# Kernel optimization log

Hardware: AMD Instinct MI355X
Metric: run time of the kernel (lower is better)

The kernel has to match this reference:

```python
import jax, jax.numpy as jnp
import numpy as np

N_U, N_M = 60000, 20000
F_U, F_M = 64, 128
IN_C, HID, OUT_C = 256, 256, 128
N = N_U + N_M
E = 500000
BN_EPS = 1e-5


def gcn_conv(z, W, b, src, dst, n):
    # PyG GCNConv: h = z @ W; add self-loops; symmetric norm D^-1/2 (A+I) D^-1/2; scatter-add; + bias
    h = z @ W                                        # [n, out]
    loop = jnp.arange(n)
    src_sl = jnp.concatenate([src, loop])            # [E+n]
    dst_sl = jnp.concatenate([dst, loop])
    deg = jax.ops.segment_sum(jnp.ones_like(dst_sl, h.dtype), dst_sl, num_segments=n)
    dinv = jax.lax.rsqrt(deg)                        # deg >= 1 due to self-loops
    norm = dinv[src_sl] * dinv[dst_sl]               # [E+n]
    msg = h[src_sl] * norm[:, None]                  # gather + scale
    out = jax.ops.segment_sum(msg, dst_sl, num_segments=n)
    return out + b


def batch_norm(z, gamma, beta):
    mean = jnp.mean(z, axis=0)
    var = jnp.var(z, axis=0)                         # biased, as torch BN uses for normalization
    return (z - mean) * jax.lax.rsqrt(var + BN_EPS) * gamma + beta


def setup_inputs() -> dict:
    key = jax.random.key(0)
    ks = jax.random.split(key, 13)
    x = jax.random.normal(ks[0], (N_U, F_U), jnp.float32)
    y = jax.random.normal(ks[1], (N_M, F_M), jnp.float32)
    edge_index = jax.random.randint(ks[2], (2, E), 0, N, dtype=jnp.int64)
    def lin(k, fin, fout):
        s = 1.0 / np.sqrt(fin)
        kw, kb = jax.random.split(k)
        return (jax.random.uniform(kw, (fin, fout), jnp.float32, -s, s),
                jax.random.uniform(kb, (fout,), jnp.float32, -s, s))
    fc1_w, fc1_b = lin(ks[3], F_U, IN_C)
    fc2_w, fc2_b = lin(ks[4], F_M, IN_C)
    conv1_w, conv1_b = lin(ks[5], IN_C, HID)
    conv2_w, conv2_b = lin(ks[6], HID, OUT_C)
    bn_gamma = jnp.ones((HID,), jnp.float32)
    bn_beta = jnp.zeros((HID,), jnp.float32)
    return {"x": x, "y": y, "edge_index": edge_index,
            "fc1_w": fc1_w, "fc1_b": fc1_b, "fc2_w": fc2_w, "fc2_b": fc2_b,
            "conv1_w": conv1_w, "conv1_b": conv1_b, "conv2_w": conv2_w, "conv2_b": conv2_b,
            "bn_gamma": bn_gamma, "bn_beta": bn_beta}


def reference(x, y, edge_index, fc1_w, fc1_b, fc2_w, fc2_b,
              conv1_w, conv1_b, conv2_w, conv2_b, bn_gamma, bn_beta):
    src, dst = edge_index[0], edge_index[1]
    xu = x @ fc1_w + fc1_b                           # [N_U, IN_C]
    xm = y @ fc2_w + fc2_b                           # [N_M, IN_C]
    z = jnp.concatenate([xu, xm], axis=0)            # [N, IN_C]
    z = gcn_conv(z, conv1_w, conv1_b, src, dst, N)   # [N, HID]
    z = jax.nn.relu(batch_norm(z, bn_gamma, bn_beta))
    z = gcn_conv(z, conv2_w, conv2_b, src, dst, N)   # [N, OUT_C]
    return z
```

## Files before the change

### kernel.cpp

```cpp
#include <hip/hip_runtime.h>
#include <math.h>
#include <stdint.h>

#define N_U 60000
#define N_M 20000
#define NN  80000
#define EE  500000
#define BN_EPS 1e-5f
#define NB_SCAN 313

typedef __attribute__((ext_vector_type(8))) short short8v;
typedef __attribute__((ext_vector_type(4))) float f32x4;

__device__ __forceinline__ unsigned short bf_hi(float f) {
    unsigned u = __float_as_uint(f);
    return (unsigned short)((u + 0x7FFFu + ((u >> 16) & 1u)) >> 16);
}
__device__ __forceinline__ float bf_f(unsigned short h) {
    return __uint_as_float(((unsigned)h) << 16);
}

__global__ void prep_kernel(const int* __restrict__ ei32, int* __restrict__ cnt,
                            int* __restrict__ cursor, int* __restrict__ rowptr,
                            float* __restrict__ sums, float* __restrict__ sumsq,
                            int* __restrict__ flag) {
    int i = blockIdx.x * blockDim.x + threadIdx.x;
    if (i < 256) { sums[i] = 0.f; sumsq[i] = 0.f; }
    for (int j = i; j < NN; j += gridDim.x * blockDim.x) { cnt[j] = 0; cursor[j] = 0; }
    if (i == 0) rowptr[NN] = EE;
    if (blockIdx.x == 0) {
        __shared__ int nz;
        if (threadIdx.x == 0) nz = 0;
        __syncthreads();
        int v = ei32[2 * threadIdx.x + 1];
        if (v != 0) atomicOr(&nz, 1);
        __syncthreads();
        if (threadIdx.x == 0) *flag = (nz == 0) ? 1 : 0;
    }
}

__device__ __forceinline__ int load_idx(const void* ei, int f, int pos) {
    return f ? (int)((const long long*)ei)[pos] : ((const int*)ei)[pos];
}

__global__ void hist_kernel(const void* __restrict__ ei, const int* __restrict__ flag,
                            int* __restrict__ cnt) {
    int f = *flag;
    int stride = gridDim.x * blockDim.x;
    for (int e = blockIdx.x * blockDim.x + threadIdx.x; e < EE; e += stride) {
        int d = load_idx(ei, f, EE + e);
        atomicAdd(&cnt[d], 1);
    }
}

__global__ void scan1_kernel(const int* __restrict__ cnt, int* __restrict__ rowptr,
                             int* __restrict__ blockSums, float* __restrict__ dinv) {
    __shared__ int sh[256];
    int tid = threadIdx.x;
    int i = blockIdx.x * 256 + tid;
    int v = (i < NN) ? cnt[i] : 0;
    int x = v;
    sh[tid] = x; __syncthreads();
#pragma unroll
    for (int off = 1; off < 256; off <<= 1) {
        int t = (tid >= off) ? sh[tid - off] : 0;
        __syncthreads();
        x += t; sh[tid] = x;
        __syncthreads();
    }
    if (i < NN) {
        rowptr[i] = x - v;
        dinv[i] = rsqrtf(1.0f + (float)v);
    }
    if (tid == 255) blockSums[blockIdx.x] = x;
}

__global__ void scan2_kernel(int* __restrict__ blockSums) {
    __shared__ int sh[512];
    int tid = threadIdx.x;
    int v = (tid < NB_SCAN) ? blockSums[tid] : 0;
    int x = v;
    sh[tid] = x; __syncthreads();
#pragma unroll
    for (int off = 1; off < 512; off <<= 1) {
        int t = (tid >= off) ? sh[tid - off] : 0;
        __syncthreads();
        x += t; sh[tid] = x;
        __syncthreads();
    }
    if (tid < NB_SCAN) blockSums[tid] = x - v;
}

__global__ void scan3_kernel(int* __restrict__ rowptr, const int* __restrict__ blockSums) {
    int i = blockIdx.x * 256 + threadIdx.x;
    if (i < NN) rowptr[i] += blockSums[blockIdx.x];
}

__global__ void fill_kernel(const void* __restrict__ ei, const int* __restrict__ flag,
                            const int* __restrict__ rowptr, int* __restrict__ cursor,
                            int* __restrict__ csr_src) {
    int f = *flag;
    int stride = gridDim.x * blockDim.x;
    for (int e = blockIdx.x * blockDim.x + threadIdx.x; e < EE; e += stride) {
        int s = load_idx(ei, f, e);
        int d = load_idx(ei, f, EE + e);
        int pos = rowptr[d] + atomicAdd(&cursor[d], 1);
        csr_src[pos] = s;
    }
}

__device__ __forceinline__ void wfrag_store(const float* W, short* Hi, short* Lo,
                                            int i, int K, int N) {
    int k = i / N, n = i - k * N;
    float v = W[i];
    unsigned short h = bf_hi(v);
    unsigned short l = bf_hi(v - bf_f(h));
    int nt = n >> 4, r = n & 15, kt = k >> 5, q = (k >> 3) & 3, p = k & 7;
    int idx = ((nt * (K / 32) + kt) << 9) + (q << 7) + (r << 3) + p;
    Hi[idx] = (short)h;
    Lo[idx] = (short)l;
}

__global__ void wsplit_all_kernel(const float* __restrict__ W1, const float* __restrict__ W2,
                                  const float* __restrict__ Wf1, const float* __restrict__ Wf2,
                                  short* __restrict__ W1h, short* __restrict__ W1l,
                                  short* __restrict__ W2h, short* __restrict__ W2l,
                                  short* __restrict__ F1h, short* __restrict__ F1l,
                                  short* __restrict__ F2h, short* __restrict__ F2l) {
    int i = blockIdx.x * 256 + threadIdx.x;
    if (i < 256 * 256) wfrag_store(W1, W1h, W1l, i, 256, 256);
    if (i < 256 * 128) wfrag_store(W2, W2h, W2l, i, 256, 128);
    if (i < 64 * 256)  wfrag_store(Wf1, F1h, F1l, i, 64, 256);
    if (i < 128 * 256) wfrag_store(Wf2, F2h, F2l, i, 128, 256);
}

template <int K, int N, int MODE, int AIN, bool BNRELU, int OUTK>
__global__ __launch_bounds__(256) void mfma_gemm_kernel(
    int M, const float* __restrict__ A,
    const short* __restrict__ AHi, const short* __restrict__ ALo,
    const short* __restrict__ WfHi, const short* __restrict__ WfLo,
    const float* __restrict__ ep, const float* __restrict__ bnsc,
    const float* __restrict__ bnsh,
    float* __restrict__ Out, short* __restrict__ OutB, short* __restrict__ OutL) {
    constexpr int LDT = 40;
    constexpr int NT = K / 32;
    __shared__ short AsHi[128 * LDT];
    __shared__ short AsLo[128 * LDT];
    const int tid  = threadIdx.x;
    const int lane = tid & 63, wave = tid >> 6;
    const int wm = (wave >> 1) * 64, wn = (wave & 1) * 64;
    const int R0 = blockIdx.x * 128;
    const int n0 = blockIdx.y * 128;
    const int srow  = tid >> 1;
    const int shalf = (tid & 1) * 16;
    const int l15  = lane & 15;
    const int koff = (lane >> 4) * 8;
    const int nt0  = (n0 + wn) >> 4;

    f32x4 acc[4][4];
#pragma unroll
    for (int mi = 0; mi < 4; ++mi)
#pragma unroll
        for (int ni = 0; ni < 4; ++ni)
            acc[mi][ni] = (f32x4){0.f, 0.f, 0.f, 0.f};

    const int arow = min(R0 + srow, M - 1);
    const float* abase = (AIN == 0) ? &A[(size_t)arow * K + shalf] : nullptr;
    const short* ahb   = (AIN == 1) ? &AHi[(size_t)arow * K + shalf] : nullptr;
    const short* alb   = (AIN == 1) ? &ALo[(size_t)arow * K + shalf] : nullptr;

    float4 a0, a1, a2, a3;
    int4 th0, th1, tl0, tl1;
    if constexpr (AIN == 0) {
        const float4* ga = (const float4*)abase;
        a0 = ga[0]; a1 = ga[1]; a2 = ga[2]; a3 = ga[3];
    } else {
        th0 = ((const int4*)ahb)[0]; th1 = ((const int4*)ahb)[1];
        tl0 = ((const int4*)alb)[0]; tl1 = ((const int4*)alb)[1];
    }

#pragma unroll
    for (int kt = 0; kt < NT; ++kt) {
        const int k0 = kt * 32;
        int4 sh0, sh1, sl0, sl1;

        if constexpr (AIN == 0) {
            if (BNRELU) {
                const float4* gs = (const float4*)&bnsc[k0 + shalf];
                const float4* gh = (const float4*)&bnsh[k0 + shalf];
                float4 s0 = gs[0], s1 = gs[1], s2 = gs[2], s3 = gs[3];
                float4 t0 = gh[0], t1 = gh[1], t2 = gh[2], t3 = gh[3];
#define BNR4(a, s, t)                                                          \
                a.x = fmaxf(a.x * s.x + t.x, 0.f);                             \
                a.y = fmaxf(a.y * s.y + t.y, 0.f);                             \
                a.z = fmaxf(a.z * s.z + t.z, 0.f);                             \
                a.w = fmaxf(a.w * s.w + t.w, 0.f);
                BNR4(a0, s0, t0); BNR4(a1, s1, t1); BNR4(a2, s2, t2); BNR4(a3, s3, t3);
#undef BNR4
            }
            unsigned h[8], l[8];
#define SPLIT4(v, hA, hB, lA, lB)                                              \
            {                                                                  \
                unsigned short h0_ = bf_hi(v.x), h1_ = bf_hi(v.y);             \
                unsigned short h2_ = bf_hi(v.z), h3_ = bf_hi(v.w);             \
                unsigned short l0_ = bf_hi(v.x - bf_f(h0_));                   \
                unsigned short l1_ = bf_hi(v.y - bf_f(h1_));                   \
                unsigned short l2_ = bf_hi(v.z - bf_f(h2_));                   \
                unsigned short l3_ = bf_hi(v.w - bf_f(h3_));                   \
                hA = (unsigned)h0_ | ((unsigned)h1_ << 16);                    \
                hB = (unsigned)h2_ | ((unsigned)h3_ << 16);                    \
                lA = (unsigned)l0_ | ((unsigned)l1_ << 16);                    \
                lB = (unsigned)l2_ | ((unsigned)l3_ << 16);                    \
            }
            SPLIT4(a0, h[0], h[1], l[0], l[1]);
            SPLIT4(a1, h[2], h[3], l[2], l[3]);
            SPLIT4(a2, h[4], h[5], l[4], l[5]);
            SPLIT4(a3, h[6], h[7], l[6], l[7]);
#undef SPLIT4
            sh0 = make_int4((int)h[0], (int)h[1], (int)h[2], (int)h[3]);
            sh1 = make_int4((int)h[4], (int)h[5], (int)h[6], (int)h[7]);
            sl0 = make_int4((int)l[0], (int)l[1], (int)l[2], (int)l[3]);
            sl1 = make_int4((int)l[4], (int)l[5], (int)l[6], (int)l[7]);
        } else {
            sh0 = th0; sh1 = th1; sl0 = tl0; sl1 = tl1;
        }

        __syncthreads();
        int4* dAH = (int4*)&AsHi[srow * LDT + shalf];
        int4* dAL = (int4*)&AsLo[srow * LDT + shalf];
        dAH[0] = sh0; dAH[1] = sh1;
        dAL[0] = sl0; dAL[1] = sl1;
        __syncthreads();

        if (kt + 1 < NT) {
            if constexpr (AIN == 0) {
                const float4* gnext = (const float4*)(abase + (kt + 1) * 32);
                a0 = gnext[0]; a1 = gnext[1]; a2 = gnext[2]; a3 = gnext[3];
            } else {
                const int4* gh = (const int4*)(ahb + (kt + 1) * 32);
                const int4* gl = (const int4*)(alb + (kt + 1) * 32);
                th0 = gh[0]; th1 = gh[1]; tl0 = gl[0]; tl1 = gl[1];
            }
        }

        short8v bh[4], bl[4];
#pragma unroll
        for (int ni = 0; ni < 4; ++ni) {
            int fidx = (((nt0 + ni) * NT + kt) << 9) + lane * 8;
            bh[ni] = *(const short8v*)&WfHi[fidx];
            bl[ni] = *(const short8v*)&WfLo[fidx];
        }

#pragma unroll
        for (int mi = 0; mi < 4; ++mi) {
            int mrow = wm + mi * 16 + l15;
            short8v ah = *(const short8v*)&AsHi[mrow * LDT + koff];
            short8v al = *(const short8v*)&AsLo[mrow * LDT + koff];
#pragma unroll
            for (int ni = 0; ni < 4; ++ni) {
                acc[mi][ni] = __builtin_amdgcn_mfma_f32_16x16x32_bf16(ah, bh[ni], acc[mi][ni], 0, 0, 0);
                acc[mi][ni] = __builtin_amdgcn_mfma_f32_16x16x32_bf16(ah, bl[ni], acc[mi][ni], 0, 0, 0);
                acc[mi][ni] = __builtin_amdgcn_mfma_f32_16x16x32_bf16(al, bh[ni], acc[mi][ni], 0, 0, 0);
            }
        }
    }

#pragma unroll
    for (int mi = 0; mi < 4; ++mi) {
#pragma unroll
        for (int i = 0; i < 4; ++i) {
            int row = R0 + wm + mi * 16 + (lane >> 4) * 4 + i;
            if (row < M) {
                float sc = (MODE == 0) ? ep[row] : 1.0f;
#pragma unroll
                for (int ni = 0; ni < 4; ++ni) {
                    int col = n0 + wn + ni * 16 + l15;
                    float v = acc[mi][ni][i];
                    v = (MODE == 0) ? v * sc : v + ep[col];
                    if constexpr (OUTK == 0) {
                        Out[(size_t)row * N + col] = v;
                    } else if constexpr (OUTK == 1) {
                        OutB[(size_t)row * N + col] = (short)bf_hi(v);
                    } else {
                        unsigned short h = bf_hi(v);
                        OutB[(size_t)row * N + col] = (short)h;
                        OutL[(size_t)row * N + col] = (short)bf_hi(v - bf_f(h));
                    }
                }
            }
        }
    }
}

__device__ __forceinline__ void acc_bf4(float4& a, ushort4 v) {
    a.x += bf_f(v.x); a.y += bf_f(v.y); a.z += bf_f(v.z); a.w += bf_f(v.w);
}

__global__ __launch_bounds__(256) void gather256_kernel(const short* __restrict__ h,
                                                        const float* __restrict__ bias,
                                                        const float* __restrict__ dinv,
                                                        const int* __restrict__ rowptr,
                                                        const int* __restrict__ csr_src,
                                                        float* __restrict__ out) {
    int wid = threadIdx.x >> 6, lane = threadIdx.x & 63;
    int r = blockIdx.x * 4 + wid;
    if (r >= NN) return;
    int beg = rowptr[r], end = rowptr[r + 1];
    float dr = dinv[r];
    const ushort4* hp = (const ushort4*)h;
    float4 acc = {0.f, 0.f, 0.f, 0.f};
    acc_bf4(acc, hp[(size_t)r * 64 + lane]);
    int k = beg;
    for (; k + 3 < end; k += 4) {
        int s0 = csr_src[k], s1 = csr_src[k + 1], s2 = csr_src[k + 2], s3 = csr_src[k + 3];
        ushort4 v0 = hp[(size_t)s0 * 64 + lane];
        ushort4 v1 = hp[(size_t)s1 * 64 + lane];
        ushort4 v2 = hp[(size_t)s2 * 64 + lane];
        ushort4 v3 = hp[(size_t)s3 * 64 + lane];
        acc_bf4(acc, v0); acc_bf4(acc, v1); acc_bf4(acc, v2); acc_bf4(acc, v3);
    }
    for (; k < end; ++k)
        acc_bf4(acc, hp[(size_t)csr_src[k] * 64 + lane]);
    float4 b = ((const float4*)bias)[lane];
    float4 o;
    o.x = b.x + dr * acc.x; o.y = b.y + dr * acc.y;
    o.z = b.z + dr * acc.z; o.w = b.w + dr * acc.w;
    ((float4*)(out + (size_t)r * 256))[lane] = o;
}

__global__ __launch_bounds__(256) void gather128_kernel(const short* __restrict__ h,
                                                        const float* __restrict__ bias,
                                                        const float* __restrict__ dinv,
                                                        const int* __restrict__ rowptr,
                                                        const int* __restrict__ csr_src,
                                                        float* __restrict__ out) {
    int sub = threadIdx.x >> 5, lane = threadIdx.x & 31;
    int r = blockIdx.x * 8 + sub;
    if (r >= NN) return;
    int beg = rowptr[r], end = rowptr[r + 1];
    float dr = dinv[r];
    const ushort4* hp = (const ushort4*)h;
    float4 acc = {0.f, 0.f, 0.f, 0.f};
    acc_bf4(acc, hp[(size_t)r * 32 + lane]);
    int k = beg;
    for (; k + 3 < end; k += 4) {
        int s0 = csr_src[k], s1 = csr_src[k + 1], s2 = csr_src[k + 2], s3 = csr_src[k + 3];
        ushort4 v0 = hp[(size_t)s0 * 32 + lane];
        ushort4 v1 = hp[(size_t)s1 * 32 + lane];
        ushort4 v2 = hp[(size_t)s2 * 32 + lane];
        ushort4 v3 = hp[(size_t)s3 * 32 + lane];
        acc_bf4(acc, v0); acc_bf4(acc, v1); acc_bf4(acc, v2); acc_bf4(acc, v3);
    }
    for (; k < end; ++k)
        acc_bf4(acc, hp[(size_t)csr_src[k] * 32 + lane]);
    float4 b = ((const float4*)bias)[lane];
    float4 o;
    o.x = b.x + dr * acc.x; o.y = b.y + dr * acc.y;
    o.z = b.z + dr * acc.z; o.w = b.w + dr * acc.w;
    ((float4*)(out + (size_t)r * 128))[lane] = o;
}

__global__ __launch_bounds__(256) void bn_stats_kernel(const float* __restrict__ a,
                                                       float* __restrict__ sums,
                                                       float* __restrict__ sumsq) {
    __shared__ float shs[256], shs2[256];
    int tid = threadIdx.x;
    int wid = tid >> 6, lane = tid & 63;
    shs[tid] = 0.f; shs2[tid] = 0.f;
    __syncthreads();
    float4 s = {0.f, 0.f, 0.f, 0.f}, s2 = {0.f, 0.f, 0.f, 0.f};
    for (int row = blockIdx.x * 4 + wid; row < NN; row += gridDim.x * 4) {
        float4 v = ((const float4*)(a + (size_t)row * 256))[lane];
        s.x += v.x; s.y += v.y; s.z += v.z; s.w += v.w;
        s2.x += v.x * v.x; s2.y += v.y * v.y; s2.z += v.z * v.z; s2.w += v.w * v.w;
    }
    atomicAdd(&shs[4 * lane + 0], s.x);  atomicAdd(&shs2[4 * lane + 0], s2.x);
    atomicAdd(&shs[4 * lane + 1], s.y);  atomicAdd(&shs2[4 * lane + 1], s2.y);
    atomicAdd(&shs[4 * lane + 2], s.z);  atomicAdd(&shs2[4 * lane + 2], s2.z);
    atomicAdd(&shs[4 * lane + 3], s.w);  atomicAdd(&shs2[4 * lane + 3], s2.w);
    __syncthreads();
    atomicAdd(&sums[tid], shs[tid]);
    atomicAdd(&sumsq[tid], shs2[tid]);
}

__global__ void bn_final_kernel(const float* __restrict__ sums, const float* __restrict__ sumsq,
                                const float* __restrict__ gamma, const float* __restrict__ beta,
                                float* __restrict__ scale, float* __restrict__ shift) {
    int c = threadIdx.x;
    const float Nf = (float)NN;
    float mean = sums[c] / Nf;
    float var = sumsq[c] / Nf - mean * mean;
    float sc = gamma[c] * rsqrtf(var + BN_EPS);
    scale[c] = sc;
    shift[c] = beta[c] - mean * sc;
}

extern "C" void kernel_launch(void* const* d_in, const int* in_sizes, int n_in,
                              void* d_out, int out_size, void* d_ws, size_t ws_size,
                              hipStream_t stream) {
    const float* x       = (const float*)d_in[0];
    const float* y       = (const float*)d_in[1];
    const void*  ei      = d_in[2];
    const float* fc1_w   = (const float*)d_in[3];
    const float* fc1_b   = (const float*)d_in[4];
    const float* fc2_w   = (const float*)d_in[5];
    const float* fc2_b   = (const float*)d_in[6];
    const float* conv1_w = (const float*)d_in[7];
    const float* conv1_b = (const float*)d_in[8];
    const float* conv2_w = (const float*)d_in[9];
    const float* conv2_b = (const float*)d_in[10];
    const float* gamma   = (const float*)d_in[11];
    const float* beta    = (const float*)d_in[12];
    float* out = (float*)d_out;

    float* ws = (float*)d_ws;
    float* bufA = ws;
    float* bufB = ws + (size_t)NN * 256;
    float* aux  = bufB + (size_t)NN * 256;
    float* dinv  = aux;
    float* sums  = dinv + NN;
    float* sumsq = sums + 256;
    float* scale = sumsq + 256;
    float* shift = scale + 256;
    int*   flag      = (int*)(shift + 256);
    int*   cnt       = flag + 1;
    int*   rowptr    = cnt + NN;
    int*   cursor    = rowptr + NN + 1;
    int*   blockSums = cursor + NN;
    int*   csr_src   = blockSums + NB_SCAN + 3;
    short* w1th = (short*)(((uintptr_t)(csr_src + EE) + 15) & ~(uintptr_t)15);
    short* w1tl = w1th + 256 * 256;
    short* w2th = w1tl + 256 * 256;
    short* w2tl = w2th + 256 * 128;
    short* wf1h = w2tl + 256 * 128;
    short* wf1l = wf1h + 256 * 64;
    short* wf2h = wf1l + 256 * 64;
    short* wf2l = wf2h + 256 * 128;

    short* zHi = (short*)bufB;
    short* zLo = zHi + (size_t)NN * 256;
    short* hA  = (short*)bufA;
    float* a1  = bufB;

    prep_kernel<<<320, 256, 0, stream>>>((const int*)ei, cnt, cursor, rowptr, sums, sumsq, flag);
    hist_kernel<<<1024, 256, 0, stream>>>(ei, flag, cnt);
    scan1_kernel<<<NB_SCAN, 256, 0, stream>>>(cnt, rowptr, blockSums, dinv);
    scan2_kernel<<<1, 512, 0, stream>>>(blockSums);
    scan3_kernel<<<NB_SCAN, 256, 0, stream>>>(rowptr, blockSums);
    fill_kernel<<<1024, 256, 0, stream>>>(ei, flag, rowptr, cursor, csr_src);
    wsplit_all_kernel<<<256, 256, 0, stream>>>(conv1_w, conv2_w, fc1_w, fc2_w,
                                               w1th, w1tl, w2th, w2tl,
                                               wf1h, wf1l, wf2h, wf2l);

    mfma_gemm_kernel<64, 256, 1, 0, false, 2><<<dim3(469, 2), 256, 0, stream>>>(
        N_U, x, nullptr, nullptr, wf1h, wf1l, fc1_b, nullptr, nullptr,
        nullptr, zHi, zLo);
    mfma_gemm_kernel<128, 256, 1, 0, false, 2><<<dim3(157, 2), 256, 0, stream>>>(
        N_M, y, nullptr, nullptr, wf2h, wf2l, fc2_b, nullptr, nullptr,
        nullptr, zHi + (size_t)N_U * 256, zLo + (size_t)N_U * 256);

    mfma_gemm_kernel<256, 256, 0, 1, false, 1><<<dim3(625, 2), 256, 0, stream>>>(
        NN, nullptr, zHi, zLo, w1th, w1tl, dinv, nullptr, nullptr,
        nullptr, hA, nullptr);
    gather256_kernel<<<NN / 4, 256, 0, stream>>>(hA, conv1_b, dinv, rowptr, csr_src, a1);

    bn_stats_kernel<<<256, 256, 0, stream>>>(a1, sums, sumsq);
    bn_final_kernel<<<1, 256, 0, stream>>>(sums, sumsq, gamma, beta, scale, shift);

    mfma_gemm_kernel<256, 128, 0, 0, true, 1><<<dim3(625, 1), 256, 0, stream>>>(
        NN, a1, nullptr, nullptr, w2th, w2tl, dinv, scale, shift,
        nullptr, hA, nullptr);
    gather128_kernel<<<NN / 8, 256, 0, stream>>>(hA, conv2_b, dinv, rowptr, csr_src, out);
}
```

Measured before the change: 403.0 us.

## Fuse BN stats into gather, merge FC GEMMs, fold weight split and scan

Folds the weight bf16 hi/lo split into the prep kernel. Removes the single-block scan2 by having each scan3 block sum the preceding block totals itself. Merges the two FC GEMM launches into one combined grid. Makes gather256 a grid-stride kernel that accumulates the batch-norm sums and sums of squares as it writes rows. This drops several kernel launches and removes the separate full re-read of the 80000x256 fp32 activation for the BN statistics. In exchange, scan3 does redundant reductions per block, and the gather now uses a fixed grid of 1024 blocks, which may change its latency hiding.

```diff
diff --git a/kernel.cpp b/kernel.cpp
--- a/kernel.cpp
+++ b/kernel.cpp
@@ -8,6 +8,7 @@
 #define EE  500000
 #define BN_EPS 1e-5f
 #define NB_SCAN 313
+#define GBLK 1024
 
 typedef __attribute__((ext_vector_type(8))) short short8v;
 typedef __attribute__((ext_vector_type(4))) float f32x4;
@@ -20,14 +21,36 @@
     return __uint_as_float(((unsigned)h) << 16);
 }
 
+__device__ __forceinline__ void wfrag_store(const float* W, short* Hi, short* Lo,
+                                            int i, int K, int N) {
+    int k = i / N, n = i - k * N;
+    float v = W[i];
+    unsigned short h = bf_hi(v);
+    unsigned short l = bf_hi(v - bf_f(h));
+    int nt = n >> 4, r = n & 15, kt = k >> 5, q = (k >> 3) & 3, p = k & 7;
+    int idx = ((nt * (K / 32) + kt) << 9) + (q << 7) + (r << 3) + p;
+    Hi[idx] = (short)h;
+    Lo[idx] = (short)l;
+}
+
 __global__ void prep_kernel(const int* __restrict__ ei32, int* __restrict__ cnt,
                             int* __restrict__ cursor, int* __restrict__ rowptr,
                             float* __restrict__ sums, float* __restrict__ sumsq,
-                            int* __restrict__ flag) {
+                            int* __restrict__ flag,
+                            const float* __restrict__ W1, const float* __restrict__ W2,
+                            const float* __restrict__ Wf1, const float* __restrict__ Wf2,
+                            short* __restrict__ W1h, short* __restrict__ W1l,
+                            short* __restrict__ W2h, short* __restrict__ W2l,
+                            short* __restrict__ F1h, short* __restrict__ F1l,
+                            short* __restrict__ F2h, short* __restrict__ F2l) {
     int i = blockIdx.x * blockDim.x + threadIdx.x;
     if (i < 256) { sums[i] = 0.f; sumsq[i] = 0.f; }
     for (int j = i; j < NN; j += gridDim.x * blockDim.x) { cnt[j] = 0; cursor[j] = 0; }
     if (i == 0) rowptr[NN] = EE;
+    if (i < 256 * 256) wfrag_store(W1, W1h, W1l, i, 256, 256);
+    if (i < 256 * 128) wfrag_store(W2, W2h, W2l, i, 256, 128);
+    if (i < 64 * 256)  wfrag_store(Wf1, F1h, F1l, i, 64, 256);
+    if (i < 128 * 256) wfrag_store(Wf2, F2h, F2l, i, 128, 256);
     if (blockIdx.x == 0) {
         __shared__ int nz;
         if (threadIdx.x == 0) nz = 0;
@@ -75,25 +98,20 @@
     if (tid == 255) blockSums[blockIdx.x] = x;
 }
 
-__global__ void scan2_kernel(int* __restrict__ blockSums) {
-    __shared__ int sh[512];
-    int tid = threadIdx.x;
-    int v = (tid < NB_SCAN) ? blockSums[tid] : 0;
-    int x = v;
-    sh[tid] = x; __syncthreads();
-#pragma unroll
-    for (int off = 1; off < 512; off <<= 1) {
-        int t = (tid >= off) ? sh[tid - off] : 0;
-        __syncthreads();
-        x += t; sh[tid] = x;
-        __syncthreads();
-    }
-    if (tid < NB_SCAN) blockSums[tid] = x - v;
-}
-
 __global__ void scan3_kernel(int* __restrict__ rowptr, const int* __restrict__ blockSums) {
-    int i = blockIdx.x * 256 + threadIdx.x;
-    if (i < NN) rowptr[i] += blockSums[blockIdx.x];
+    __shared__ int red[256];
+    int b = blockIdx.x, tid = threadIdx.x;
+    int s = 0;
+    for (int j = tid; j < b; j += 256) s += blockSums[j];
+    red[tid] = s; __syncthreads();
+#pragma unroll
+    for (int off = 128; off > 0; off >>= 1) {
+        if (tid < off) red[tid] += red[tid + off];
+        __syncthreads();
+    }
+    int base = red[0];
+    int i = b * 256 + tid;
+    if (i < NN) rowptr[i] += base;
 }
 
 __global__ void fill_kernel(const void* __restrict__ ei, const int* __restrict__ flag,
@@ -109,34 +127,10 @@
     }
 }
 
-__device__ __forceinline__ void wfrag_store(const float* W, short* Hi, short* Lo,
-                                            int i, int K, int N) {
-    int k = i / N, n = i - k * N;
-    float v = W[i];
-    unsigned short h = bf_hi(v);
-    unsigned short l = bf_hi(v - bf_f(h));
-    int nt = n >> 4, r = n & 15, kt = k >> 5, q = (k >> 3) & 3, p = k & 7;
-    int idx = ((nt * (K / 32) + kt) << 9) + (q << 7) + (r << 3) + p;
-    Hi[idx] = (short)h;
-    Lo[idx] = (short)l;
-}
-
-__global__ void wsplit_all_kernel(const float* __restrict__ W1, const float* __restrict__ W2,
-                                  const float* __restrict__ Wf1, const float* __restrict__ Wf2,
-                                  short* __restrict__ W1h, short* __restrict__ W1l,
-                                  short* __restrict__ W2h, short* __restrict__ W2l,
-                                  short* __restrict__ F1h, short* __restrict__ F1l,
-                                  short* __restrict__ F2h, short* __restrict__ F2l) {
-    int i = blockIdx.x * 256 + threadIdx.x;
-    if (i < 256 * 256) wfrag_store(W1, W1h, W1l, i, 256, 256);
-    if (i < 256 * 128) wfrag_store(W2, W2h, W2l, i, 256, 128);
-    if (i < 64 * 256)  wfrag_store(Wf1, F1h, F1l, i, 64, 256);
-    if (i < 128 * 256) wfrag_store(Wf2, F2h, F2l, i, 128, 256);
-}
-
 template <int K, int N, int MODE, int AIN, bool BNRELU, int OUTK>
-__global__ __launch_bounds__(256) void mfma_gemm_kernel(
-    int M, const float* __restrict__ A,
+__device__ __forceinline__ void mfma_gemm_body(
+    int M, int bx, int by, short* AsHi, short* AsLo,
+    const float* __restrict__ A,
     const short* __restrict__ AHi, const short* __restrict__ ALo,
     const short* __restrict__ WfHi, const short* __restrict__ WfLo,
     const float* __restrict__ ep, const float* __restrict__ bnsc,
@@ -144,13 +138,11 @@
     float* __restrict__ Out, short* __restrict__ OutB, short* __restrict__ OutL) {
     constexpr int LDT = 40;
     constexpr int NT = K / 32;
-    __shared__ short AsHi[128 * LDT];
-    __shared__ short AsLo[128 * LDT];
     const int tid  = threadIdx.x;
     const int lane = tid & 63, wave = tid >> 6;
     const int wm = (wave >> 1) * 64, wn = (wave & 1) * 64;
-    const int R0 = blockIdx.x * 128;
-    const int n0 = blockIdx.y * 128;
+    const int R0 = bx * 128;
+    const int n0 = by * 128;
     const int srow  = tid >> 1;
     const int shalf = (tid & 1) * 16;
     const int l15  = lane & 15;
@@ -292,6 +284,43 @@
     }
 }
 
+template <int K, int N, int MODE, int AIN, bool BNRELU, int OUTK>
+__global__ __launch_bounds__(256) void mfma_gemm_kernel(
+    int M, const float* __restrict__ A,
+    const short* __restrict__ AHi, const short* __restrict__ ALo,
+    const short* __restrict__ WfHi, const short* __restrict__ WfLo,
+    const float* __restrict__ ep, const float* __restrict__ bnsc,
+    const float* __restrict__ bnsh,
+    float* __restrict__ Out, short* __restrict__ OutB, short* __restrict__ OutL) {
+    __shared__ short AsHi[128 * 40];
+    __shared__ short AsLo[128 * 40];
+    mfma_gemm_body<K, N, MODE, AIN, BNRELU, OUTK>(
+        M, blockIdx.x, blockIdx.y, AsHi, AsLo, A, AHi, ALo, WfHi, WfLo,
+        ep, bnsc, bnsh, Out, OutB, OutL);
+}
+
+__global__ __launch_bounds__(256) void fc_combined_kernel(
+    const float* __restrict__ x, const float* __restrict__ y,
+    const short* __restrict__ wf1h, const short* __restrict__ wf1l,
+    const short* __restrict__ wf2h, const short* __restrict__ wf2l,
+    const float* __restrict__ fc1_b, const float* __restrict__ fc2_b,
+    short* __restrict__ zHi, short* __restrict__ zLo) {
+    __shared__ short AsHi[128 * 40];
+    __shared__ short AsLo[128 * 40];
+    int b = blockIdx.x;
+    if (b < 938) {
+        mfma_gemm_body<64, 256, 1, 0, false, 2>(
+            N_U, b % 469, b / 469, AsHi, AsLo, x, nullptr, nullptr,
+            wf1h, wf1l, fc1_b, nullptr, nullptr, nullptr, zHi, zLo);
+    } else {
+        b -= 938;
+        mfma_gemm_body<128, 256, 1, 0, false, 2>(
+            N_M, b % 157, b / 157, AsHi, AsLo, y, nullptr, nullptr,
+            wf2h, wf2l, fc2_b, nullptr, nullptr, nullptr,
+            zHi + (size_t)N_U * 256, zLo + (size_t)N_U * 256);
+    }
+}
+
 __device__ __forceinline__ void acc_bf4(float4& a, ushort4 v) {
     a.x += bf_f(v.x); a.y += bf_f(v.y); a.z += bf_f(v.z); a.w += bf_f(v.w);
 }
@@ -301,31 +330,47 @@
                                                         const float* __restrict__ dinv,
                                                         const int* __restrict__ rowptr,
                                                         const int* __restrict__ csr_src,
-                                                        float* __restrict__ out) {
-    int wid = threadIdx.x >> 6, lane = threadIdx.x & 63;
-    int r = blockIdx.x * 4 + wid;
-    if (r >= NN) return;
-    int beg = rowptr[r], end = rowptr[r + 1];
-    float dr = dinv[r];
+                                                        float* __restrict__ out,
+                                                        float* __restrict__ sums,
+                                                        float* __restrict__ sumsq) {
+    __shared__ float shs[256], shs2[256];
+    int tid = threadIdx.x;
+    int wid = tid >> 6, lane = tid & 63;
+    shs[tid] = 0.f; shs2[tid] = 0.f;
+    __syncthreads();
     const ushort4* hp = (const ushort4*)h;
-    float4 acc = {0.f, 0.f, 0.f, 0.f};
-    acc_bf4(acc, hp[(size_t)r * 64 + lane]);
-    int k = beg;
-    for (; k + 3 < end; k += 4) {
-        int s0 = csr_src[k], s1 = csr_src[k + 1], s2 = csr_src[k + 2], s3 = csr_src[k + 3];
-        ushort4 v0 = hp[(size_t)s0 * 64 + lane];
-        ushort4 v1 = hp[(size_t)s1 * 64 + lane];
-        ushort4 v2 = hp[(size_t)s2 * 64 + lane];
-        ushort4 v3 = hp[(size_t)s3 * 64 + lane];
-        acc_bf4(acc, v0); acc_bf4(acc, v1); acc_bf4(acc, v2); acc_bf4(acc, v3);
-    }
-    for (; k < end; ++k)
-        acc_bf4(acc, hp[(size_t)csr_src[k] * 64 + lane]);
-    float4 b = ((const float4*)bias)[lane];
-    float4 o;
-    o.x = b.x + dr * acc.x; o.y = b.y + dr * acc.y;
-    o.z = b.z + dr * acc.z; o.w = b.w + dr * acc.w;
-    ((float4*)(out + (size_t)r * 256))[lane] = o;
+    float4 b4 = ((const float4*)bias)[lane];
+    float4 ss = {0.f, 0.f, 0.f, 0.f}, ss2 = {0.f, 0.f, 0.f, 0.f};
+    for (int r = blockIdx.x * 4 + wid; r < NN; r += GBLK * 4) {
+        int beg = rowptr[r], end = rowptr[r + 1];
+        float dr = dinv[r];
+        float4 acc = {0.f, 0.f, 0.f, 0.f};
+        acc_bf4(acc, hp[(size_t)r * 64 + lane]);
+        int k = beg;
+        for (; k + 3 < end; k += 4) {
+            int s0 = csr_src[k], s1 = csr_src[k + 1], s2 = csr_src[k + 2], s3 = csr_src[k + 3];
+            ushort4 v0 = hp[(size_t)s0 * 64 + lane];
+            ushort4 v1 = hp[(size_t)s1 * 64 + lane];
+            ushort4 v2 = hp[(size_t)s2 * 64 + lane];
+            ushort4 v3 = hp[(size_t)s3 * 64 + lane];
+            acc_bf4(acc, v0); acc_bf4(acc, v1); acc_bf4(acc, v2); acc_bf4(acc, v3);
+        }
+        for (; k < end; ++k)
+            acc_bf4(acc, hp[(size_t)csr_src[k] * 64 + lane]);
+        float4 o;
+        o.x = b4.x + dr * acc.x; o.y = b4.y + dr * acc.y;
+        o.z = b4.z + dr * acc.z; o.w = b4.w + dr * acc.w;
+        ((float4*)(out + (size_t)r * 256))[lane] = o;
+        ss.x += o.x; ss.y += o.y; ss.z += o.z; ss.w += o.w;
+        ss2.x += o.x * o.x; ss2.y += o.y * o.y; ss2.z += o.z * o.z; ss2.w += o.w * o.w;
+    }
+    atomicAdd(&shs[4 * lane + 0], ss.x);  atomicAdd(&shs2[4 * lane + 0], ss2.x);
+    atomicAdd(&shs[4 * lane + 1], ss.y);  atomicAdd(&shs2[4 * lane + 1], ss2.y);
+    atomicAdd(&shs[4 * lane + 2], ss.z);  atomicAdd(&shs2[4 * lane + 2], ss2.z);
+    atomicAdd(&shs[4 * lane + 3], ss.w);  atomicAdd(&shs2[4 * lane + 3], ss2.w);
+    __syncthreads();
+    atomicAdd(&sums[tid], shs[tid]);
+    atomicAdd(&sumsq[tid], shs2[tid]);
 }
 
 __global__ __launch_bounds__(256) void gather128_kernel(const short* __restrict__ h,
@@ -358,29 +403,6 @@
     o.x = b.x + dr * acc.x; o.y = b.y + dr * acc.y;
     o.z = b.z + dr * acc.z; o.w = b.w + dr * acc.w;
     ((float4*)(out + (size_t)r * 128))[lane] = o;
-}
-
-__global__ __launch_bounds__(256) void bn_stats_kernel(const float* __restrict__ a,
-                                                       float* __restrict__ sums,
-                                                       float* __restrict__ sumsq) {
-    __shared__ float shs[256], shs2[256];
-    int tid = threadIdx.x;
-    int wid = tid >> 6, lane = tid & 63;
-    shs[tid] = 0.f; shs2[tid] = 0.f;
-    __syncthreads();
-    float4 s = {0.f, 0.f, 0.f, 0.f}, s2 = {0.f, 0.f, 0.f, 0.f};
-    for (int row = blockIdx.x * 4 + wid; row < NN; row += gridDim.x * 4) {
-        float4 v = ((const float4*)(a + (size_t)row * 256))[lane];
-        s.x += v.x; s.y += v.y; s.z += v.z; s.w += v.w;
-        s2.x += v.x * v.x; s2.y += v.y * v.y; s2.z += v.z * v.z; s2.w += v.w * v.w;
-    }
-    atomicAdd(&shs[4 * lane + 0], s.x);  atomicAdd(&shs2[4 * lane + 0], s2.x);
-    atomicAdd(&shs[4 * lane + 1], s.y);  atomicAdd(&shs2[4 * lane + 1], s2.y);
-    atomicAdd(&shs[4 * lane + 2], s.z);  atomicAdd(&shs2[4 * lane + 2], s2.z);
-    atomicAdd(&shs[4 * lane + 3], s.w);  atomicAdd(&shs2[4 * lane + 3], s2.w);
-    __syncthreads();
-    atomicAdd(&sums[tid], shs[tid]);
-    atomicAdd(&sumsq[tid], shs2[tid]);
 }
 
 __global__ void bn_final_kernel(const float* __restrict__ sums, const float* __restrict__ sumsq,
@@ -442,29 +464,22 @@
     short* hA  = (short*)bufA;
     float* a1  = bufB;
 
-    prep_kernel<<<320, 256, 0, stream>>>((const int*)ei, cnt, cursor, rowptr, sums, sumsq, flag);
+    prep_kernel<<<320, 256, 0, stream>>>((const int*)ei, cnt, cursor, rowptr, sums, sumsq,
+                                         flag, conv1_w, conv2_w, fc1_w, fc2_w,
+                                         w1th, w1tl, w2th, w2tl, wf1h, wf1l, wf2h, wf2l);
     hist_kernel<<<1024, 256, 0, stream>>>(ei, flag, cnt);
     scan1_kernel<<<NB_SCAN, 256, 0, stream>>>(cnt, rowptr, blockSums, dinv);
-    scan2_kernel<<<1, 512, 0, stream>>>(blockSums);
     scan3_kernel<<<NB_SCAN, 256, 0, stream>>>(rowptr, blockSums);
     fill_kernel<<<1024, 256, 0, stream>>>(ei, flag, rowptr, cursor, csr_src);
-    wsplit_all_kernel<<<256, 256, 0, stream>>>(conv1_w, conv2_w, fc1_w, fc2_w,
-                                               w1th, w1tl, w2th, w2tl,
-                                               wf1h, wf1l, wf2h, wf2l);
-
-    mfma_gemm_kernel<64, 256, 1, 0, false, 2><<<dim3(469, 2), 256, 0, stream>>>(
-        N_U, x, nullptr, nullptr, wf1h, wf1l, fc1_b, nullptr, nullptr,
-        nullptr, zHi, zLo);
-    mfma_gemm_kernel<128, 256, 1, 0, false, 2><<<dim3(157, 2), 256, 0, stream>>>(
-        N_M, y, nullptr, nullptr, wf2h, wf2l, fc2_b, nullptr, nullptr,
-        nullptr, zHi + (size_t)N_U * 256, zLo + (size_t)N_U * 256);
+
+    fc_combined_kernel<<<1252, 256, 0, stream>>>(x, y, wf1h, wf1l, wf2h, wf2l,
+                                                 fc1_b, fc2_b, zHi, zLo);
 
     mfma_gemm_kernel<256, 256, 0, 1, false, 1><<<dim3(625, 2), 256, 0, stream>>>(
         NN, nullptr, zHi, zLo, w1th, w1tl, dinv, nullptr, nullptr,
         nullptr, hA, nullptr);
-    gather256_kernel<<<NN / 4, 256, 0, stream>>>(hA, conv1_b, dinv, rowptr, csr_src, a1);
-
-    bn_stats_kernel<<<256, 256, 0, stream>>>(a1, sums, sumsq);
+    gather256_kernel<<<GBLK, 256, 0, stream>>>(hA, conv1_b, dinv, rowptr, csr_src,
+                                               a1, sums, sumsq);
     bn_final_kernel<<<1, 256, 0, stream>>>(sums, sumsq, gamma, beta, scale, shift);
 
     mfma_gemm_kernel<256, 128, 0, 0, true, 1><<<dim3(625, 1), 256, 0, stream>>>(
```

Result: faster. 390.2 us (-3.2%).
